# Kernel optimization log

Hardware: AMD Instinct MI355X
Metric: run time of the kernel (lower is better)

The kernel has to match this reference:

```python
import jax, jax.numpy as jnp
import numpy as np

N = 100000      # nodes
E = 1600000     # edges (before self-loops)
IN = 256        # in_channels
H = 4           # heads (layer 1)
C = 16          # hidden_channels
OUT = 40        # out_channels
NEG_SLOPE = 0.2  # PyG GATConv default


def setup_inputs() -> dict:
    key = jax.random.key(0)
    ks = jax.random.split(key, 10)
    x = jax.random.normal(ks[0], (N, IN), dtype=jnp.float32)
    edge_index = jax.random.randint(ks[1], (2, E), 0, N, dtype=jnp.int64)
    s = 0.1
    return {
        "x": x,
        "edge_index": edge_index,
        "W1": jax.random.normal(ks[2], (IN, H * C), dtype=jnp.float32) * s,
        "a_src1": jax.random.normal(ks[3], (H, C), dtype=jnp.float32) * s,
        "a_dst1": jax.random.normal(ks[4], (H, C), dtype=jnp.float32) * s,
        "b1": jnp.zeros((H * C,), dtype=jnp.float32),
        "W2": jax.random.normal(ks[5], (H * C, OUT), dtype=jnp.float32) * s,
        "a_src2": jax.random.normal(ks[6], (1, OUT), dtype=jnp.float32) * s,
        "a_dst2": jax.random.normal(ks[7], (1, OUT), dtype=jnp.float32) * s,
        "b2": jnp.zeros((OUT,), dtype=jnp.float32),
    }


def gat_conv(x, src, dst, W, a_s, a_d, b, heads, ch, n):
    # x: [n, d_in] -> projected [n, heads, ch]
    xp = (x @ W).reshape(n, heads, ch)
    # per-node attention contributions [n, heads]
    e_s = jnp.einsum('nhc,hc->nh', xp, a_s)
    e_d = jnp.einsum('nhc,hc->nh', xp, a_d)
    # per-edge logits (gather) [E, heads]
    e = jax.nn.leaky_relu(e_s[src] + e_d[dst], negative_slope=NEG_SLOPE)
    # segment softmax over edges sharing a destination node
    m = jax.ops.segment_max(e, dst, num_segments=n)
    m = jnp.where(jnp.isfinite(m), m, 0.0)
    ex = jnp.exp(e - m[dst])
    z = jax.ops.segment_sum(ex, dst, num_segments=n)
    alpha = ex / (z[dst] + 1e-16)               # [E, heads]
    # weighted scatter-add aggregation [n, heads, ch]
    out = jax.ops.segment_sum(xp[src] * alpha[:, :, None], dst, num_segments=n)
    return out.reshape(n, heads * ch) + b       # concat heads + bias


def reference(x, edge_index, W1, a_src1, a_dst1, b1, W2, a_src2, a_dst2, b2):
    n = x.shape[0]
    loop = jnp.arange(n, dtype=edge_index.dtype)
    src = jnp.concatenate([edge_index[0], loop])  # PyG add_self_loops=True
    dst = jnp.concatenate([edge_index[1], loop])
    h = gat_conv(x, src, dst, W1, a_src1, a_dst1, b1, H, C, n)
    h = jax.nn.relu(h)
    out = gat_conv(h, src, dst, W2, a_src2, a_dst2, b2, 1, OUT, n)
    return out
```

## Files before the change

kernel.cpp:

```cpp
#include <hip/hip_runtime.h>
#include <hip/hip_bf16.h>

#define IN_DIM 256
#define HC     64
#define OUT_DIM 40
#define NEG    0.2f

#define NB_SH   8
#define NB_MASK 255
#define SRC_BITS 17
#define SRC_MASK 0x1FFFF
#define CHUNK   8192
#define LEN_CAP 6144

typedef __bf16 bf16x8 __attribute__((ext_vector_type(8)));
typedef float  f32x4  __attribute__((ext_vector_type(4)));

__device__ inline float lrelu(float v) { return fmaxf(v, NEG * v); }

__global__ __launch_bounds__(256) void hist_kernel(
    const int* __restrict__ ei, int* __restrict__ blkhist, int E, int ET, int nbuck) {
  __shared__ int hist[512];
  int tid = threadIdx.x;
  for (int i = tid; i < nbuck; i += 256) hist[i] = 0;
  __syncthreads();
  int base = blockIdx.x * CHUNK;
  #pragma unroll 4
  for (int it = 0; it < CHUNK / 256; ++it) {
    int e = base + it * 256 + tid;
    if (e < ET) {
      int d = (e < E) ? ei[E + e] : (e - E);
      atomicAdd(&hist[d >> NB_SH], 1);
    }
  }
  __syncthreads();
  for (int i = tid; i < nbuck; i += 256) blkhist[blockIdx.x * nbuck + i] = hist[i];
}

__global__ __launch_bounds__(256) void bsum_kernel(
    const int* __restrict__ blkhist, int* __restrict__ btot, int nblk, int nbuck) {
  __shared__ int sm[256];
  int b = blockIdx.x, tid = threadIdx.x;
  int s = 0;
  for (int i = tid; i < nblk; i += 256) s += blkhist[(size_t)i * nbuck + b];
  sm[tid] = s; __syncthreads();
  #pragma unroll
  for (int o = 128; o; o >>= 1) {
    if (tid < o) sm[tid] += sm[tid + o];
    __syncthreads();
  }
  if (tid == 0) btot[b] = sm[0];
}

__global__ __launch_bounds__(512) void bscan_kernel(
    const int* __restrict__ btot, int* __restrict__ bstart,
    int* __restrict__ offs, int nbuck, int ET, int n) {
  __shared__ int sm[512];
  int tid = threadIdx.x;
  int total = (tid < nbuck) ? btot[tid] : 0;
  sm[tid] = total; __syncthreads();
  for (int o = 1; o < 512; o <<= 1) {
    int v = (tid >= o) ? sm[tid - o] : 0;
    __syncthreads();
    sm[tid] += v;
    __syncthreads();
  }
  if (tid < nbuck) bstart[tid] = sm[tid] - total;
  if (tid == 0) { bstart[nbuck] = ET; offs[n] = ET; }
}

__global__ __launch_bounds__(256) void curs_kernel(
    const int* __restrict__ blkhist, const int* __restrict__ bstart,
    int* __restrict__ cur, int nblk, int nbuck) {
  __shared__ int sm[256];
  int b = blockIdx.x, tid = threadIdx.x;
  int run = bstart[b];
  for (int c = 0; c < nblk; c += 256) {
    int idx = c + tid;
    int v = (idx < nblk) ? blkhist[(size_t)idx * nbuck + b] : 0;
    sm[tid] = v; __syncthreads();
    for (int o = 1; o < 256; o <<= 1) {
      int x = (tid >= o) ? sm[tid - o] : 0;
      __syncthreads();
      sm[tid] += x;
      __syncthreads();
    }
    if (idx < nblk) cur[(size_t)idx * nbuck + b] = run + sm[tid] - v;
    run += sm[255];
    __syncthreads();
  }
}

__global__ __launch_bounds__(512) void scatter1_kernel(
    const int* __restrict__ ei, const int* __restrict__ cur,
    unsigned int* __restrict__ pairs, int E, int ET, int nbuck) {
  __shared__ int hs[512];
  __shared__ int addb[512];
  __shared__ int lcnt[512];
  __shared__ unsigned int lout[CHUNK];
  __shared__ int ldst[CHUNK];
  int tid = threadIdx.x, blk = blockIdx.x, base = blk * CHUNK;
  hs[tid] = 0; lcnt[tid] = 0;
  __syncthreads();
  int se[16], de[16];
  #pragma unroll
  for (int it = 0; it < CHUNK / 512; ++it) {
    int e = base + it * 512 + tid;
    int s = 0, d = 0;
    if (e < ET) {
      if (e < E) { s = ei[e]; d = ei[E + e]; }
      else       { s = e - E; d = s; }
      atomicAdd(&hs[d >> NB_SH], 1);
    }
    se[it] = s; de[it] = d;
  }
  __syncthreads();
  int t = hs[tid];
  for (int o = 1; o < 512; o <<= 1) {
    int v = (tid >= o) ? hs[tid - o] : 0;
    __syncthreads();
    hs[tid] += v;
    __syncthreads();
  }
  int lofs = hs[tid] - t;
  __syncthreads();
  hs[tid] = lofs;
  addb[tid] = ((tid < nbuck) ? cur[(size_t)blk * nbuck + tid] : 0) - lofs;
  __syncthreads();
  #pragma unroll
  for (int it = 0; it < CHUNK / 512; ++it) {
    int e = base + it * 512 + tid;
    if (e < ET) {
      int b = de[it] >> NB_SH;
      int pos = hs[b] + atomicAdd(&lcnt[b], 1);
      lout[pos] = (unsigned)se[it] | ((unsigned)(de[it] & NB_MASK) << SRC_BITS);
      ldst[pos] = addb[b] + pos;
    }
  }
  __syncthreads();
  int len = min(CHUNK, ET - base);
  for (int i = tid; i < len; i += 512) pairs[ldst[i]] = lout[i];
}

__global__ __launch_bounds__(512) void place2_kernel(
    const unsigned int* __restrict__ pairs, const int* __restrict__ bstart,
    int* __restrict__ offs, int* __restrict__ srcs, int n, int nbuck) {
  __shared__ unsigned int lin[LEN_CAP];
  __shared__ unsigned int lou[LEN_CAP];
  __shared__ int lhs[256];
  __shared__ int lcnt[256];
  __shared__ int sm[512];
  int b = blockIdx.x, tid = threadIdx.x;
  int rbeg = bstart[b], rend = bstart[b + 1], len = rend - rbeg;
  int node0 = b << NB_SH;
  int nloc = min(256, n - node0);
  if (tid < 256) { lhs[tid] = 0; lcnt[tid] = 0; }
  __syncthreads();
  if (len <= LEN_CAP) {
    for (int i = tid; i < len; i += 512) {
      unsigned p = pairs[rbeg + i];
      lin[i] = p;
      atomicAdd(&lhs[(p >> SRC_BITS) & NB_MASK], 1);
    }
    __syncthreads();
    int t = (tid < 256) ? lhs[tid] : 0;
    sm[tid] = t; __syncthreads();
    for (int o = 1; o < 512; o <<= 1) {
      int v = (tid >= o) ? sm[tid - o] : 0;
      __syncthreads();
      sm[tid] += v;
      __syncthreads();
    }
    int excl = sm[tid] - t;
    if (tid < nloc) offs[node0 + tid] = rbeg + excl;
    if (tid < 256) lhs[tid] = excl;
    __syncthreads();
    for (int i = tid; i < len; i += 512) {
      unsigned p = lin[i];
      int dl = (p >> SRC_BITS) & NB_MASK;
      int pos = lhs[dl] + atomicAdd(&lcnt[dl], 1);
      lou[pos] = p & SRC_MASK;
    }
    __syncthreads();
    for (int i = tid; i < len; i += 512) srcs[rbeg + i] = (int)lou[i];
  } else {
    for (int i = tid; i < len; i += 512)
      atomicAdd(&lhs[(pairs[rbeg + i] >> SRC_BITS) & NB_MASK], 1);
    __syncthreads();
    int t = (tid < 256) ? lhs[tid] : 0;
    sm[tid] = t; __syncthreads();
    for (int o = 1; o < 512; o <<= 1) {
      int v = (tid >= o) ? sm[tid - o] : 0;
      __syncthreads();
      sm[tid] += v;
      __syncthreads();
    }
    int excl = sm[tid] - t;
    if (tid < nloc) offs[node0 + tid] = rbeg + excl;
    if (tid < 256) lhs[tid] = excl;
    __syncthreads();
    for (int i = tid; i < len; i += 512) {
      unsigned p = pairs[rbeg + i];
      int dl = (p >> SRC_BITS) & NB_MASK;
      int pos = lhs[dl] + atomicAdd(&lcnt[dl], 1);
      srcs[rbeg + pos] = (int)(p & SRC_MASK);
    }
  }
}

__global__ void wprep_kernel(const float* __restrict__ W1, __bf16* __restrict__ Wt) {
  int i = blockIdx.x * blockDim.x + threadIdx.x;
  if (i >= IN_DIM * HC) return;
  int k = i >> 6, nn = i & 63;
  Wt[nn * IN_DIM + k] = (__bf16)W1[i];
}

__global__ __launch_bounds__(256, 4) void gemm1_mfma(
    const float* __restrict__ x, const __bf16* __restrict__ Wt,
    const float* __restrict__ a_s, const float* __restrict__ a_d,
    __bf16* __restrict__ xp1b, float* __restrict__ es1, float* __restrict__ ed1, int n) {
  __shared__ uint4 wl[2048];
  int tid = threadIdx.x;
  const uint4* gw = (const uint4*)Wt;
  #pragma unroll
  for (int it = 0; it < 8; ++it) {
    int c16 = it * 256 + tid;
    int row = c16 >> 5;
    int swz = c16 ^ (row & 7);
    wl[swz] = gw[c16];
  }
  __syncthreads();

  int wave = tid >> 6, lane = tid & 63;
  int l15 = lane & 15, kgrp = lane >> 4;
  int rowA = blockIdx.x * 64 + wave * 16 + l15;
  bool okA = rowA < n;
  const float* xrow = x + (size_t)(okA ? rowA : (n - 1)) * IN_DIM;

  f32x4 va[8][2];
  #pragma unroll
  for (int c = 0; c < 8; ++c) {
    int k0 = c * 32 + kgrp * 8;
    va[c][0] = *(const f32x4*)(xrow + k0);
    va[c][1] = *(const f32x4*)(xrow + k0 + 4);
  }
  __builtin_amdgcn_sched_barrier(0);

  f32x4 acc[4] = {};
  #pragma unroll
  for (int c = 0; c < 8; ++c) {
    bf16x8 ahi, alo;
    #pragma unroll
    for (int i = 0; i < 4; ++i) {
      float f0 = va[c][0][i], f1 = va[c][1][i];
      __bf16 h0 = (__bf16)f0, h1 = (__bf16)f1;
      ahi[i]     = h0;
      ahi[4 + i] = h1;
      alo[i]     = (__bf16)(f0 - (float)h0);
      alo[4 + i] = (__bf16)(f1 - (float)h1);
    }
    #pragma unroll
    for (int t = 0; t < 4; ++t) {
      int row  = t * 16 + l15;
      int unit = row * 32 + c * 4 + kgrp;
      int swz  = unit ^ (row & 7);
      bf16x8 b = *(const bf16x8*)&wl[swz];
      acc[t] = __builtin_amdgcn_mfma_f32_16x16x32_bf16(ahi, b, acc[t], 0, 0, 0);
      acc[t] = __builtin_amdgcn_mfma_f32_16x16x32_bf16(alo, b, acc[t], 0, 0, 0);
    }
  }

  int rowbase = blockIdx.x * 64 + wave * 16 + kgrp * 4;
  #pragma unroll
  for (int t = 0; t < 4; ++t) {
    float as_v = a_s[t * 16 + l15], ad_v = a_d[t * 16 + l15];
    #pragma unroll
    for (int r = 0; r < 4; ++r) {
      int row = rowbase + r;
      float v = acc[t][r];
      bool ok = row < n;
      if (ok) xp1b[(size_t)row * HC + t * 16 + l15] = (__bf16)v;
      float ps = v * as_v, pd = v * ad_v;
      #pragma unroll
      for (int o = 1; o < 16; o <<= 1) {
        ps += __shfl_xor(ps, o, 16);
        pd += __shfl_xor(pd, o, 16);
      }
      if (ok && l15 == 0) {
        es1[row * 4 + t] = ps;
        ed1[row * 4 + t] = pd;
      }
    }
  }
}

__global__ __launch_bounds__(256) void agg1_csr(
    const int* __restrict__ offs, const int* __restrict__ srcs,
    const float* __restrict__ es1, const float* __restrict__ ed1,
    const __bf16* __restrict__ xp1b, const float* __restrict__ b1,
    __bf16* __restrict__ hb, int n) {
  __shared__ float lds[4][16 * 4 * 2];
  int wave = threadIdx.x >> 6;
  int wid = (blockIdx.x * 256 + threadIdx.x) >> 6;
  if (wid >= n) return;
  int lane = threadIdx.x & 63;
  int eidx = lane >> 2, hA = lane & 3;
  int a = lane & 31, half = lane >> 5;
  int ch0 = a * 2, headB = a >> 3;
  int beg = offs[wid], end = offs[wid + 1];
  float edh = ed1[wid * 4 + hA];
  float zacc = 0.f, acc0 = 0.f, acc1 = 0.f;
  const char* xbase = (const char*)xp1b + ch0 * 2;
  float* myl = lds[wave];

  for (int e0 = beg; e0 < end; e0 += 16) {
    int cnt = min(16, end - e0);
    float ex = 0.f;
    int s = 0;
    if (eidx < cnt) {
      s = srcs[e0 + eidx];
      ex = __expf(lrelu(es1[s * 4 + hA] + edh));
    }
    zacc += ex;
    myl[lane * 2]     = ex;
    myl[lane * 2 + 1] = __int_as_float(s * (int)(HC * sizeof(__bf16)));
    if (cnt == 16) {
      float2 ao[8];
      #pragma unroll
      for (int jp = 0; jp < 8; ++jp)
        ao[jp] = *(const float2*)&myl[((jp * 2 + half) * 4 + headB) * 2];
      unsigned wj[8];
      #pragma unroll
      for (int jp = 0; jp < 8; ++jp)
        wj[jp] = *(const unsigned*)(xbase + __float_as_int(ao[jp].y));
      #pragma unroll
      for (int jp = 0; jp < 8; ++jp) {
        float f0 = __int_as_float((int)(wj[jp] << 16));
        float f1 = __int_as_float((int)(wj[jp] & 0xffff0000u));
        acc0 = fmaf(ao[jp].x, f0, acc0);
        acc1 = fmaf(ao[jp].x, f1, acc1);
      }
    } else {
      int jpmax = (cnt + 1 - half) >> 1;
      #pragma unroll 4
      for (int jp = 0; jp < jpmax; ++jp) {
        float2 ao = *(const float2*)&myl[((jp * 2 + half) * 4 + headB) * 2];
        unsigned w = *(const unsigned*)(xbase + __float_as_int(ao.y));
        float f0 = __int_as_float((int)(w << 16));
        float f1 = __int_as_float((int)(w & 0xffff0000u));
        acc0 = fmaf(ao.x, f0, acc0);
        acc1 = fmaf(ao.x, f1, acc1);
      }
    }
  }

  float z = zacc;
  z += __shfl_xor(z, 4); z += __shfl_xor(z, 8);
  z += __shfl_xor(z, 16); z += __shfl_xor(z, 32);
  float zc = __shfl(z, headB);
  acc0 += __shfl_xor(acc0, 32);
  acc1 += __shfl_xor(acc1, 32);
  if (half == 0) {
    float inv = 1.f / (zc + 1e-16f);
    __bf16 r0 = (__bf16)fmaxf(fmaf(acc0, inv, b1[ch0]), 0.f);
    __bf16 r1 = (__bf16)fmaxf(fmaf(acc1, inv, b1[ch0 + 1]), 0.f);
    unsigned pk = ((unsigned)*(unsigned short*)&r0) |
                  (((unsigned)*(unsigned short*)&r1) << 16);
    *(unsigned*)&hb[(size_t)wid * HC + ch0] = pk;
  }
}

__global__ __launch_bounds__(256) void layer2_mfma(
    const __bf16* __restrict__ hb, const float* __restrict__ W2,
    const float* __restrict__ a_s2, const float* __restrict__ a_d2,
    __bf16* __restrict__ xp2b, float* __restrict__ es2, float* __restrict__ ed2, int n) {
  int tid = threadIdx.x;
  int wave = tid >> 6, lane = tid & 63;
  int l15 = lane & 15, kgrp = lane >> 4;
  int rowA = blockIdx.x * 64 + wave * 16 + l15;
  const __bf16* hrow = hb + (size_t)(rowA < n ? rowA : (n - 1)) * HC;

  bf16x8 av[2];
  av[0] = *(const bf16x8*)(hrow + kgrp * 8);
  av[1] = *(const bf16x8*)(hrow + 32 + kgrp * 8);

  f32x4 acc[3] = {};
  #pragma unroll
  for (int c = 0; c < 2; ++c) {
    #pragma unroll
    for (int t = 0; t < 3; ++t) {
      int col = t * 16 + l15;
      bool okc = col < OUT_DIM;
      bf16x8 bhi, blo;
      #pragma unroll
      for (int i = 0; i < 8; ++i) {
        int k = c * 32 + kgrp * 8 + i;
        float w = okc ? W2[k * OUT_DIM + col] : 0.f;
        __bf16 wh = (__bf16)w;
        bhi[i] = wh;
        blo[i] = (__bf16)(w - (float)wh);
      }
      acc[t] = __builtin_amdgcn_mfma_f32_16x16x32_bf16(av[c], bhi, acc[t], 0, 0, 0);
      acc[t] = __builtin_amdgcn_mfma_f32_16x16x32_bf16(av[c], blo, acc[t], 0, 0, 0);
    }
  }

  int rowbase = blockIdx.x * 64 + wave * 16 + kgrp * 4;
  #pragma unroll
  for (int r = 0; r < 4; ++r) {
    int row = rowbase + r;
    bool ok = row < n;
    float ps = 0.f, pd = 0.f;
    #pragma unroll
    for (int t = 0; t < 3; ++t) {
      int col = t * 16 + l15;
      if (col < OUT_DIM) {
        float v = acc[t][r];
        if (ok) xp2b[(size_t)row * OUT_DIM + col] = (__bf16)v;
        ps = fmaf(v, a_s2[col], ps);
        pd = fmaf(v, a_d2[col], pd);
      }
    }
    #pragma unroll
    for (int o = 1; o < 16; o <<= 1) {
      ps += __shfl_xor(ps, o, 16);
      pd += __shfl_xor(pd, o, 16);
    }
    if (ok && l15 == 0) { es2[row] = ps; ed2[row] = pd; }
  }
}

__global__ __launch_bounds__(256) void agg2_csr(
    const int* __restrict__ offs, const int* __restrict__ srcs,
    const float* __restrict__ es2, const float* __restrict__ ed2,
    const __bf16* __restrict__ xp2b, const float* __restrict__ b2,
    float* __restrict__ out, int n) {
  __shared__ float lds[4][64 * 2];
  int wave = threadIdx.x >> 6;
  int wid = (blockIdx.x * 256 + threadIdx.x) >> 6;
  if (wid >= n) return;
  int lane = threadIdx.x & 63;
  int a = lane & 31, half = lane >> 5;
  int ch0 = a * 2;
  int beg = offs[wid], end = offs[wid + 1];
  float edv = ed2[wid];
  float zacc = 0.f, acc0 = 0.f, acc1 = 0.f;
  const char* xbase = (const char*)xp2b + ch0 * 2;
  float* myl = lds[wave];

  for (int e0 = beg; e0 < end; e0 += 64) {
    int cnt = min(64, end - e0);
    float ex = 0.f;
    int s = 0;
    if (lane < cnt) {
      s = srcs[e0 + lane];
      ex = __expf(lrelu(es2[s] + edv));
    }
    zacc += ex;
    myl[lane * 2]     = ex;
    myl[lane * 2 + 1] = __int_as_float(s * (int)(OUT_DIM * sizeof(__bf16)));
    if (a < 20) {
      int jpmax = (cnt + 1 - half) >> 1;
      int jp = 0;
      for (; jp + 8 <= jpmax; jp += 8) {
        float2 ao[8];
        #pragma unroll
        for (int k = 0; k < 8; ++k)
          ao[k] = *(const float2*)&myl[((jp + k) * 2 + half) * 2];
        unsigned wj[8];
        #pragma unroll
        for (int k = 0; k < 8; ++k)
          wj[k] = *(const unsigned*)(xbase + __float_as_int(ao[k].y));
        #pragma unroll
        for (int k = 0; k < 8; ++k) {
          float f0 = __int_as_float((int)(wj[k] << 16));
          float f1 = __int_as_float((int)(wj[k] & 0xffff0000u));
          acc0 = fmaf(ao[k].x, f0, acc0);
          acc1 = fmaf(ao[k].x, f1, acc1);
        }
      }
      #pragma unroll 4
      for (; jp < jpmax; ++jp) {
        float2 ao = *(const float2*)&myl[(jp * 2 + half) * 2];
        unsigned w = *(const unsigned*)(xbase + __float_as_int(ao.y));
        float f0 = __int_as_float((int)(w << 16));
        float f1 = __int_as_float((int)(w & 0xffff0000u));
        acc0 = fmaf(ao.x, f0, acc0);
        acc1 = fmaf(ao.x, f1, acc1);
      }
    }
  }

  float z = zacc;
  #pragma unroll
  for (int o = 1; o < 64; o <<= 1) z += __shfl_xor(z, o);
  acc0 += __shfl_xor(acc0, 32);
  acc1 += __shfl_xor(acc1, 32);
  if (half == 0 && a < 20) {
    float inv = 1.f / (z + 1e-16f);
    float2 r;
    r.x = fmaf(acc0, inv, b2[ch0]);
    r.y = fmaf(acc1, inv, b2[ch0 + 1]);
    *(float2*)&out[(size_t)wid * OUT_DIM + ch0] = r;
  }
}

extern "C" void kernel_launch(void* const* d_in, const int* in_sizes, int n_in,
                              void* d_out, int out_size, void* d_ws, size_t ws_size,
                              hipStream_t stream) {
  const float* x    = (const float*)d_in[0];
  const int*   ei   = (const int*)d_in[1];
  const float* W1   = (const float*)d_in[2];
  const float* a_s1 = (const float*)d_in[3];
  const float* a_d1 = (const float*)d_in[4];
  const float* b1   = (const float*)d_in[5];
  const float* W2   = (const float*)d_in[6];
  const float* a_s2 = (const float*)d_in[7];
  const float* a_d2 = (const float*)d_in[8];
  const float* b2   = (const float*)d_in[9];

  int n  = in_sizes[0] / IN_DIM;
  int E  = in_sizes[1] / 2;
  int ET = E + n;
  int nbuck = (n + 255) >> NB_SH;
  int nblk1 = (ET + CHUNK - 1) / CHUNK;
  float* out = (float*)d_out;

  char* ws = (char*)d_ws;
  size_t off = 0;
  auto alloc = [&](size_t bytes) -> void* {
    void* p = ws + off;
    off = (off + bytes + 255) & ~(size_t)255;
    return p;
  };
  __bf16* xp1b    = (__bf16*)alloc((size_t)n * HC * 2);
  __bf16* xp2b    = (__bf16*)alloc((size_t)n * OUT_DIM * 2);
  __bf16* hb      = (__bf16*)alloc((size_t)n * HC * 2);
  float*  es1     = (float*)alloc((size_t)n * 4 * 4);
  float*  ed1     = (float*)alloc((size_t)n * 4 * 4);
  float*  es2     = (float*)alloc((size_t)n * 4);
  float*  ed2     = (float*)alloc((size_t)n * 4);
  int*    blkhist = (int*)alloc((size_t)nblk1 * nbuck * 4);
  int*    cur     = (int*)alloc((size_t)nblk1 * nbuck * 4);
  int*    btot    = (int*)alloc((size_t)(nbuck + 1) * 4);
  int*    bstart  = (int*)alloc((size_t)(nbuck + 1) * 4);
  int*    offs    = (int*)alloc((size_t)(n + 1) * 4);
  int*    srcs    = (int*)alloc((size_t)ET * 4);
  unsigned int* pairs = (unsigned int*)alloc((size_t)ET * 4);
  __bf16* Wt      = (__bf16*)alloc((size_t)IN_DIM * HC * 2);

  hist_kernel<<<nblk1, 256, 0, stream>>>(ei, blkhist, E, ET, nbuck);
  bsum_kernel<<<nbuck, 256, 0, stream>>>(blkhist, btot, nblk1, nbuck);
  bscan_kernel<<<1, 512, 0, stream>>>(btot, bstart, offs, nbuck, ET, n);
  curs_kernel<<<nbuck, 256, 0, stream>>>(blkhist, bstart, cur, nblk1, nbuck);
  scatter1_kernel<<<nblk1, 512, 0, stream>>>(ei, cur, pairs, E, ET, nbuck);
  place2_kernel<<<nbuck, 512, 0, stream>>>(pairs, bstart, offs, srcs, n, nbuck);

  wprep_kernel<<<(IN_DIM * HC + 255) / 256, 256, 0, stream>>>(W1, Wt);
  gemm1_mfma<<<(n + 63) / 64, 256, 0, stream>>>(x, Wt, a_s1, a_d1,
                                                xp1b, es1, ed1, n);
  agg1_csr<<<(n * 64 + 255) / 256, 256, 0, stream>>>(offs, srcs, es1, ed1, xp1b, b1, hb, n);
  layer2_mfma<<<(n + 63) / 64, 256, 0, stream>>>(hb, W2, a_s2, a_d2, xp2b, es2, ed2, n);
  agg2_csr<<<(n * 64 + 255) / 256, 256, 0, stream>>>(offs, srcs, es2, ed2, xp2b, b2, out, n);
}
```

Before: 196.6 us.

## Fold bucket-total reduction into histogram kernel and vectorize edge-index loads

Removes the separate bucket-sum kernel. The histogram kernel now adds its per-block counts straight into the bucket totals with global atomics, and the totals are zeroed inside the weight-prep kernel, which is moved to the start of the stream. The per-block histogram is stored transposed so the cursor-scan kernel reads each bucket's row with coalesced accesses. The histogram and scatter kernels load edge indices as int4 vectors, which changes which edges each thread handles. The cost is extra global atomic traffic on the bucket totals and a dependency on the weight-prep kernel running first.

```diff
diff --git a/kernel.cpp b/kernel.cpp
--- a/kernel.cpp
+++ b/kernel.cpp
@@ -19,37 +19,39 @@
 __device__ inline float lrelu(float v) { return fmaxf(v, NEG * v); }
 
 __global__ __launch_bounds__(256) void hist_kernel(
-    const int* __restrict__ ei, int* __restrict__ blkhist, int E, int ET, int nbuck) {
+    const int* __restrict__ ei, int* __restrict__ blkhistT, int* __restrict__ btot,
+    int E, int ET, int nbuck, int nblk) {
   __shared__ int hist[512];
   int tid = threadIdx.x;
-  for (int i = tid; i < nbuck; i += 256) hist[i] = 0;
+  hist[tid] = 0; hist[tid + 256] = 0;
   __syncthreads();
   int base = blockIdx.x * CHUNK;
-  #pragma unroll 4
-  for (int it = 0; it < CHUNK / 256; ++it) {
-    int e = base + it * 256 + tid;
-    if (e < ET) {
-      int d = (e < E) ? ei[E + e] : (e - E);
-      atomicAdd(&hist[d >> NB_SH], 1);
-    }
-  }
-  __syncthreads();
-  for (int i = tid; i < nbuck; i += 256) blkhist[blockIdx.x * nbuck + i] = hist[i];
-}
-
-__global__ __launch_bounds__(256) void bsum_kernel(
-    const int* __restrict__ blkhist, int* __restrict__ btot, int nblk, int nbuck) {
-  __shared__ int sm[256];
-  int b = blockIdx.x, tid = threadIdx.x;
-  int s = 0;
-  for (int i = tid; i < nblk; i += 256) s += blkhist[(size_t)i * nbuck + b];
-  sm[tid] = s; __syncthreads();
-  #pragma unroll
-  for (int o = 128; o; o >>= 1) {
-    if (tid < o) sm[tid] += sm[tid + o];
-    __syncthreads();
-  }
-  if (tid == 0) btot[b] = sm[0];
+  #pragma unroll
+  for (int it = 0; it < CHUNK / 1024; ++it) {
+    int e = base + it * 1024 + tid * 4;
+    if (e + 3 < E) {
+      int4 d4 = *(const int4*)&ei[E + e];
+      atomicAdd(&hist[d4.x >> NB_SH], 1);
+      atomicAdd(&hist[d4.y >> NB_SH], 1);
+      atomicAdd(&hist[d4.z >> NB_SH], 1);
+      atomicAdd(&hist[d4.w >> NB_SH], 1);
+    } else {
+      #pragma unroll
+      for (int k = 0; k < 4; ++k) {
+        int ee = e + k;
+        if (ee < ET) {
+          int d = (ee < E) ? ei[E + ee] : (ee - E);
+          atomicAdd(&hist[d >> NB_SH], 1);
+        }
+      }
+    }
+  }
+  __syncthreads();
+  for (int i = tid; i < nbuck; i += 256) {
+    int c = hist[i];
+    blkhistT[(size_t)i * nblk + blockIdx.x] = c;
+    if (c) atomicAdd(&btot[i], c);
+  }
 }
 
 __global__ __launch_bounds__(512) void bscan_kernel(
@@ -70,14 +72,14 @@
 }
 
 __global__ __launch_bounds__(256) void curs_kernel(
-    const int* __restrict__ blkhist, const int* __restrict__ bstart,
+    const int* __restrict__ blkhistT, const int* __restrict__ bstart,
     int* __restrict__ cur, int nblk, int nbuck) {
   __shared__ int sm[256];
   int b = blockIdx.x, tid = threadIdx.x;
   int run = bstart[b];
   for (int c = 0; c < nblk; c += 256) {
     int idx = c + tid;
-    int v = (idx < nblk) ? blkhist[(size_t)idx * nbuck + b] : 0;
+    int v = (idx < nblk) ? blkhistT[(size_t)b * nblk + idx] : 0;
     sm[tid] = v; __syncthreads();
     for (int o = 1; o < 256; o <<= 1) {
       int x = (tid >= o) ? sm[tid - o] : 0;
@@ -104,15 +106,28 @@
   __syncthreads();
   int se[16], de[16];
   #pragma unroll
-  for (int it = 0; it < CHUNK / 512; ++it) {
-    int e = base + it * 512 + tid;
-    int s = 0, d = 0;
-    if (e < ET) {
-      if (e < E) { s = ei[e]; d = ei[E + e]; }
-      else       { s = e - E; d = s; }
-      atomicAdd(&hs[d >> NB_SH], 1);
-    }
-    se[it] = s; de[it] = d;
+  for (int it = 0; it < CHUNK / 2048; ++it) {
+    int e = base + it * 2048 + tid * 4;
+    if (e + 3 < E) {
+      int4 s4 = *(const int4*)&ei[e];
+      int4 d4 = *(const int4*)&ei[E + e];
+      se[it * 4 + 0] = s4.x; de[it * 4 + 0] = d4.x; atomicAdd(&hs[d4.x >> NB_SH], 1);
+      se[it * 4 + 1] = s4.y; de[it * 4 + 1] = d4.y; atomicAdd(&hs[d4.y >> NB_SH], 1);
+      se[it * 4 + 2] = s4.z; de[it * 4 + 2] = d4.z; atomicAdd(&hs[d4.z >> NB_SH], 1);
+      se[it * 4 + 3] = s4.w; de[it * 4 + 3] = d4.w; atomicAdd(&hs[d4.w >> NB_SH], 1);
+    } else {
+      #pragma unroll
+      for (int k = 0; k < 4; ++k) {
+        int ee = e + k;
+        int s = 0, d = 0;
+        if (ee < ET) {
+          if (ee < E) { s = ei[ee]; d = ei[E + ee]; }
+          else        { s = ee - E; d = s; }
+          atomicAdd(&hs[d >> NB_SH], 1);
+        }
+        se[it * 4 + k] = s; de[it * 4 + k] = d;
+      }
+    }
   }
   __syncthreads();
   int t = hs[tid];
@@ -128,13 +143,17 @@
   addb[tid] = ((tid < nbuck) ? cur[(size_t)blk * nbuck + tid] : 0) - lofs;
   __syncthreads();
   #pragma unroll
-  for (int it = 0; it < CHUNK / 512; ++it) {
-    int e = base + it * 512 + tid;
-    if (e < ET) {
-      int b = de[it] >> NB_SH;
-      int pos = hs[b] + atomicAdd(&lcnt[b], 1);
-      lout[pos] = (unsigned)se[it] | ((unsigned)(de[it] & NB_MASK) << SRC_BITS);
-      ldst[pos] = addb[b] + pos;
+  for (int it = 0; it < CHUNK / 2048; ++it) {
+    #pragma unroll
+    for (int k = 0; k < 4; ++k) {
+      int e = base + it * 2048 + tid * 4 + k;
+      if (e < ET) {
+        int b = de[it * 4 + k] >> NB_SH;
+        int pos = hs[b] + atomicAdd(&lcnt[b], 1);
+        lout[pos] = (unsigned)se[it * 4 + k] |
+                    ((unsigned)(de[it * 4 + k] & NB_MASK) << SRC_BITS);
+        ldst[pos] = addb[b] + pos;
+      }
     }
   }
   __syncthreads();
@@ -208,8 +227,10 @@
   }
 }
 
-__global__ void wprep_kernel(const float* __restrict__ W1, __bf16* __restrict__ Wt) {
+__global__ void wprep_kernel(const float* __restrict__ W1, __bf16* __restrict__ Wt,
+                             int* __restrict__ btot, int nbuck) {
   int i = blockIdx.x * blockDim.x + threadIdx.x;
+  if (i < nbuck) btot[i] = 0;
   if (i >= IN_DIM * HC) return;
   int k = i >> 6, nn = i & 63;
   Wt[nn * IN_DIM + k] = (__bf16)W1[i];
@@ -533,30 +554,29 @@
     off = (off + bytes + 255) & ~(size_t)255;
     return p;
   };
-  __bf16* xp1b    = (__bf16*)alloc((size_t)n * HC * 2);
-  __bf16* xp2b    = (__bf16*)alloc((size_t)n * OUT_DIM * 2);
-  __bf16* hb      = (__bf16*)alloc((size_t)n * HC * 2);
-  float*  es1     = (float*)alloc((size_t)n * 4 * 4);
-  float*  ed1     = (float*)alloc((size_t)n * 4 * 4);
-  float*  es2     = (float*)alloc((size_t)n * 4);
-  float*  ed2     = (float*)alloc((size_t)n * 4);
-  int*    blkhist = (int*)alloc((size_t)nblk1 * nbuck * 4);
-  int*    cur     = (int*)alloc((size_t)nblk1 * nbuck * 4);
-  int*    btot    = (int*)alloc((size_t)(nbuck + 1) * 4);
-  int*    bstart  = (int*)alloc((size_t)(nbuck + 1) * 4);
-  int*    offs    = (int*)alloc((size_t)(n + 1) * 4);
-  int*    srcs    = (int*)alloc((size_t)ET * 4);
+  __bf16* xp1b     = (__bf16*)alloc((size_t)n * HC * 2);
+  __bf16* xp2b     = (__bf16*)alloc((size_t)n * OUT_DIM * 2);
+  __bf16* hb       = (__bf16*)alloc((size_t)n * HC * 2);
+  float*  es1      = (float*)alloc((size_t)n * 4 * 4);
+  float*  ed1      = (float*)alloc((size_t)n * 4 * 4);
+  float*  es2      = (float*)alloc((size_t)n * 4);
+  float*  ed2      = (float*)alloc((size_t)n * 4);
+  int*    blkhistT = (int*)alloc((size_t)nblk1 * nbuck * 4);
+  int*    cur      = (int*)alloc((size_t)nblk1 * nbuck * 4);
+  int*    btot     = (int*)alloc((size_t)(nbuck + 1) * 4);
+  int*    bstart   = (int*)alloc((size_t)(nbuck + 1) * 4);
+  int*    offs     = (int*)alloc((size_t)(n + 1) * 4);
+  int*    srcs     = (int*)alloc((size_t)ET * 4);
   unsigned int* pairs = (unsigned int*)alloc((size_t)ET * 4);
-  __bf16* Wt      = (__bf16*)alloc((size_t)IN_DIM * HC * 2);
-
-  hist_kernel<<<nblk1, 256, 0, stream>>>(ei, blkhist, E, ET, nbuck);
-  bsum_kernel<<<nbuck, 256, 0, stream>>>(blkhist, btot, nblk1, nbuck);
+  __bf16* Wt       = (__bf16*)alloc((size_t)IN_DIM * HC * 2);
+
+  wprep_kernel<<<(IN_DIM * HC + 255) / 256, 256, 0, stream>>>(W1, Wt, btot, nbuck);
+  hist_kernel<<<nblk1, 256, 0, stream>>>(ei, blkhistT, btot, E, ET, nbuck, nblk1);
   bscan_kernel<<<1, 512, 0, stream>>>(btot, bstart, offs, nbuck, ET, n);
-  curs_kernel<<<nbuck, 256, 0, stream>>>(blkhist, bstart, cur, nblk1, nbuck);
+  curs_kernel<<<nbuck, 256, 0, stream>>>(blkhistT, bstart, cur, nblk1, nbuck);
   scatter1_kernel<<<nblk1, 512, 0, stream>>>(ei, cur, pairs, E, ET, nbuck);
   place2_kernel<<<nbuck, 512, 0, stream>>>(pairs, bstart, offs, srcs, n, nbuck);
 
-  wprep_kernel<<<(IN_DIM * HC + 255) / 256, 256, 0, stream>>>(W1, Wt);
   gemm1_mfma<<<(n + 63) / 64, 256, 0, stream>>>(x, Wt, a_s1, a_d1,
                                                 xp1b, es1, ed1, n);
   agg1_csr<<<(n * 64 + 255) / 256, 256, 0, stream>>>(offs, srcs, es1, ed1, xp1b, b1, hb, n);
```

After: 194.9 us. No clear change (-0.9%).
